# Performance work log

Hardware: AMD Instinct MI355X
Metric: run time of the kernel (lower is better)

Reference implementation:

```python
import jax, jax.numpy as jnp
import numpy as np

NHEAD = 8
DILATED = 1


def setup_inputs() -> dict:
    key = jax.random.key(0)
    ks = jax.random.split(key, 5)
    bs, c, h, w, k = 2, 256, 128, 128, 8
    L = (h // 2) * (w // 2)
    return {
        "query": jax.random.normal(ks[0], (bs, c, h, w), jnp.float32),
        "key": jax.random.normal(ks[1], (bs, c, h, w), jnp.float32),
        "value": jax.random.normal(ks[2], (bs, c, h, w), jnp.float32),
        "topk_pos": jax.random.randint(ks[3], (bs, L, k, 2), 0, h // 2, dtype=jnp.int32).astype(jnp.int64),
        "rel_pos": jax.random.normal(ks[4], (bs, NHEAD, h, w, 4 * k), jnp.float32),
    }


def reference(query, key, value, topk_pos, rel_pos):
    bs, c, h0, w0 = query.shape
    h1, w1 = key.shape[2], key.shape[3]
    nh = NHEAD
    d = c // nh
    L = (h0 // 2) * (w0 // 2)
    k = topk_pos.shape[2]
    k4 = 4 * k

    # key/value: [b,c,h,w] -> [b, h1*w1, nh, d]
    kf = key.reshape(bs, c, h1 * w1).transpose(0, 2, 1).reshape(bs, h1 * w1, nh, d)
    vf = value.reshape(bs, c, h1 * w1).transpose(0, 2, 1).reshape(bs, h1 * w1, nh, d)

    # query grouped into 2x2 blocks: [b, L, 4, nh, d]
    q = query.reshape(bs, nh, d, h0 // 2, 2, w0 // 2, 2)
    q = q.transpose(0, 3, 5, 4, 6, 1, 2).reshape(bs, L, 4, nh, d)

    # build gather indices into flattened key grid (offsets by dilation)
    tp = topk_pos * 2                               # [b, L, k, 2]
    row, col = tp[..., 0], tp[..., 1]
    offs = [(0, 0), (0, DILATED), (DILATED, 0), (DILATED, DILATED)]
    idx = jnp.stack([(row + x) * w1 + (col + y) for x, y in offs], axis=3)  # [b,L,k,4]
    idx = jnp.clip(idx, 0, h1 * w1 - 1).reshape(bs, L, k4)

    def gather(tbl):  # tbl: [b, h1*w1, nh, d] -> [b, L, k4, nh, d]
        return jax.vmap(lambda t, i: t[i])(tbl, idx.reshape(bs, L * k4)).reshape(bs, L, k4, nh, d)

    kg = gather(kf)
    vg = gather(vf)

    scale = 1.0 / np.sqrt(d).astype(np.float32)
    qk = jnp.einsum('blthd,blmhd->bltmh', q, kg) * scale  # [b,L,4,k4,nh]

    rp = rel_pos.reshape(bs, nh, h0 // 2, 2, w0 // 2, 2, k4)
    rp = rp.transpose(0, 2, 4, 3, 5, 6, 1).reshape(bs, L, 4, k4, nh)
    qk = qk + rp

    A = jax.nn.softmax(qk, axis=-2)  # softmax over the k*4 candidate axis
    msg = jnp.einsum('bltmh,blmhd->blthd', A, vg)  # [b,L,4,nh,d]

    # un-group 2x2 blocks back to full resolution: [b, h0*w0, c]
    msg = msg.reshape(bs, h0 // 2, w0 // 2, 2, 2, nh, d)
    msg = msg.transpose(0, 1, 3, 2, 4, 5, 6).reshape(bs, h0 * w0, c)

    up_idx = jnp.broadcast_to(idx[:, :, None, :], (bs, L, 4, k4))
    up_idx = up_idx.reshape(bs, h0 // 2, w0 // 2, 2, 2, k4)
    up_idx = up_idx.transpose(0, 1, 3, 2, 4, 5).reshape(bs, h0 * w0, k4)
    return msg, up_idx
```

## Files before the change

kernel.cpp:

```cpp
#include <hip/hip_runtime.h>
#include <hip/hip_fp16.h>
#include <math.h>

constexpr int NH = 8;
constexpr int D = 32;
constexpr int C = 256;
constexpr int H0 = 128;
constexpr int W0 = 128;
constexpr int PIX = H0 * W0;
constexpr int LBLK = 4096;
constexpr int K4 = 32;
constexpr int KSTH = 260;
constexpr int KST = 258;

typedef _Float16 half2_t __attribute__((ext_vector_type(2)));

#if defined(__has_builtin)
#if __has_builtin(__builtin_amdgcn_fdot2)
#define HAVE_FDOT2 1
#endif
#endif

__device__ __forceinline__ float fdot2_acc(half2_t a, half2_t b, float c) {
#ifdef HAVE_FDOT2
  return __builtin_amdgcn_fdot2(a, b, c, false);
#else
  return c + (float)a.x * (float)b.x + (float)a.y * (float)b.y;
#endif
}

__global__ __launch_bounds__(256) void transpose_qkv_kernel(
    const float* __restrict__ q, const float* __restrict__ k,
    const float* __restrict__ v, __half* __restrict__ qT,
    __half* __restrict__ kT, __half* __restrict__ vT)
{
  __shared__ float tile[64 * 65];
  const int z = blockIdx.z;
  const int b = z & 1;
  const int arr = z >> 1;
  const float* src = (arr == 0 ? q : arr == 1 ? k : v) + (size_t)b * C * PIX;
  __half* dst = (arr == 0 ? qT : arr == 1 ? kT : vT) + (size_t)b * PIX * C;

  const int p0 = blockIdx.x * 64;
  const int c0 = blockIdx.y * 64;
  const int t15 = threadIdx.x & 15;
  const int thi4 = threadIdx.x >> 4;

#pragma unroll
  for (int r = 0; r < 4; ++r) {
    const int ch = thi4 + r * 16;
    const int p4 = t15 * 4;
    float4 f = *(const float4*)&src[(size_t)(c0 + ch) * PIX + p0 + p4];
    tile[(p4 + 0) * 65 + ch] = f.x;
    tile[(p4 + 1) * 65 + ch] = f.y;
    tile[(p4 + 2) * 65 + ch] = f.z;
    tile[(p4 + 3) * 65 + ch] = f.w;
  }
  __syncthreads();

  const int t7 = threadIdx.x & 7;
  const int th8 = threadIdx.x >> 3;
#pragma unroll
  for (int r = 0; r < 2; ++r) {
    const int p = th8 + r * 32;
    const int c8 = t7 * 8;
    const float* tr = &tile[p * 65 + c8];
    __half2 h0 = __floats2half2_rn(tr[0], tr[1]);
    __half2 h1 = __floats2half2_rn(tr[2], tr[3]);
    __half2 h2 = __floats2half2_rn(tr[4], tr[5]);
    __half2 h3 = __floats2half2_rn(tr[6], tr[7]);
    uint4 u;
    u.x = *(unsigned*)&h0; u.y = *(unsigned*)&h1;
    u.z = *(unsigned*)&h2; u.w = *(unsigned*)&h3;
    *(uint4*)&dst[(size_t)(p0 + p) * C + c0 + c8] = u;
  }
}

__global__ __launch_bounds__(256) void cascade_attn_f16(
    const __half* __restrict__ qT,
    const __half* __restrict__ kT,
    const __half* __restrict__ vT,
    const int* __restrict__ topk,
    const float* __restrict__ relp,
    float* __restrict__ out_msg,
    float* __restrict__ out_idx)
{
  __shared__ __half kvh[K4 * KSTH];
  __shared__ __half qph[4 * C];

  const int tid = threadIdx.x;
  const int bid = blockIdx.x;
  const int b = bid >> 12;
  const int l = bid & (LBLK - 1);
  const int by = l >> 6, bx = l & 63;
  const int r0 = by * 2, c0 = bx * 2;

  const int* tp = topk + ((size_t)b * LBLK + l) * 16;

  const int h = tid >> 5;
  const int m = tid & 31;

  {
    const int t = tid >> 6, ln = tid & 63;
    const int pix = r0 * W0 + c0 + (t >> 1) * W0 + (t & 1);
    uint2 f = *(const uint2*)&qT[((size_t)b * PIX + pix) * C + ln * 4];
    *(uint2*)&qph[t * C + ln * 4] = f;
  }

  const int p = tid >> 3;
  const int ln8 = tid & 7;
  const int jj = p >> 2, o = p & 3;
  const int gpix = (tp[jj * 2] * 2 + (o >> 1)) * W0 + tp[jj * 2 + 1] * 2 + (o & 1);

  {
    const __half* src = &kT[((size_t)b * PIX + gpix) * C + ln8 * 8];
#pragma unroll
    for (int i = 0; i < 4; ++i) {
      uint4 f = *(const uint4*)(src + i * 64);
      __half* dst = &kvh[p * KSTH + ln8 * 8 + i * 64];
      *(uint2*)dst = make_uint2(f.x, f.y);
      *(uint2*)(dst + 4) = make_uint2(f.z, f.w);
    }
  }

  uint4 vreg[4];
  {
    const __half* src = &vT[((size_t)b * PIX + gpix) * C + ln8 * 8];
#pragma unroll
    for (int i = 0; i < 4; ++i) vreg[i] = *(const uint4*)(src + i * 64);
  }

  const size_t rb = ((((size_t)b * NH + h) * H0 + r0) * W0 + c0) * K4 + m;
  float rl0 = relp[rb];
  float rl1 = relp[rb + K4];
  float rl2 = relp[rb + (size_t)W0 * K4];
  float rl3 = relp[rb + (size_t)W0 * K4 + K4];

  if (tid < 128) {
    const int mm = tid & 31, t = tid >> 5;
    const int j2 = mm >> 2, o2 = mm & 3;
    const int pix = (tp[j2 * 2] * 2 + (o2 >> 1)) * W0 + tp[j2 * 2 + 1] * 2 + (o2 & 1);
    const int prow = r0 + (t >> 1), pcol = c0 + (t & 1);
    out_idx[((size_t)b * PIX + prow * W0 + pcol) * K4 + mm] = (float)pix;
  }
  __syncthreads();

  uint2 kw[8];
  {
    const __half* kbase = &kvh[m * KSTH + h * D];
#pragma unroll
    for (int i = 0; i < 8; ++i) kw[i] = *(const uint2*)(kbase + i * 4);
  }
  const half2_t* kh = (const half2_t*)kw;

  float acc[4] = {0.f, 0.f, 0.f, 0.f};
#pragma unroll
  for (int t = 0; t < 4; ++t) {
    uint4 qw[2];
    const uint4* qf = (const uint4*)&qph[t * C + h * D];
    qw[0] = qf[0];
    qw[1] = qf[1];
    const half2_t* qh2 = (const half2_t*)qw;
    uint4 qw2[2];
    qw2[0] = qf[2];
    qw2[1] = qf[3];
    const half2_t* qh2b = (const half2_t*)qw2;
#pragma unroll
    for (int i = 0; i < 8; ++i) acc[t] = fdot2_acc(qh2[i], kh[i], acc[t]);
#pragma unroll
    for (int i = 0; i < 8; ++i) acc[t] = fdot2_acc(qh2b[i], kh[8 + i], acc[t]);
  }

  const float scale = 0.17677669529663687f;
  float sv[4];
  sv[0] = acc[0] * scale + rl0;
  sv[1] = acc[1] * scale + rl1;
  sv[2] = acc[2] * scale + rl2;
  sv[3] = acc[3] * scale + rl3;

  float pr4[4];
#pragma unroll
  for (int t = 0; t < 4; ++t) {
    float x = sv[t];
    float mx = x;
#pragma unroll
    for (int off = 16; off > 0; off >>= 1) mx = fmaxf(mx, __shfl_xor(mx, off));
    float pbit = __expf(x - mx);
    float sm = pbit;
#pragma unroll
    for (int off = 16; off > 0; off >>= 1) sm += __shfl_xor(sm, off);
    pr4[t] = pbit / sm;
  }
  __syncthreads();

  {
    __half2 p01 = __floats2half2_rn(pr4[0], pr4[1]);
    __half2 p23 = __floats2half2_rn(pr4[2], pr4[3]);
    uint2 u;
    u.x = *(unsigned*)&p01;
    u.y = *(unsigned*)&p23;
    *(uint2*)&qph[tid * 4] = u;
  }
#pragma unroll
  for (int i = 0; i < 4; ++i) {
    __half* dst = &kvh[p * KSTH + ln8 * 8 + i * 64];
    *(uint2*)dst = make_uint2(vreg[i].x, vreg[i].y);
    *(uint2*)(dst + 4) = make_uint2(vreg[i].z, vreg[i].w);
  }
  __syncthreads();

  float o0 = 0.f, o1 = 0.f, o2 = 0.f, o3 = 0.f;
#pragma unroll
  for (int mm = 0; mm < 32; ++mm) {
    uint2 au = *(const uint2*)&qph[(h * K4 + mm) * 4];
    __half2 a01 = *(__half2*)&au.x;
    __half2 a23 = *(__half2*)&au.y;
    float2 f01 = __half22float2(a01);
    float2 f23 = __half22float2(a23);
    float vv = __half2float(kvh[mm * KSTH + h * D + m]);
    o0 += f01.x * vv;
    o1 += f01.y * vv;
    o2 += f23.x * vv;
    o3 += f23.y * vv;
  }
  const size_t ob = ((size_t)b * PIX + (size_t)r0 * W0 + c0) * C + h * D + m;
  out_msg[ob] = o0;
  out_msg[ob + C] = o1;
  out_msg[ob + (size_t)W0 * C] = o2;
  out_msg[ob + (size_t)W0 * C + C] = o3;
}

__global__ __launch_bounds__(256) void cascade_attn_fallback(
    const float* __restrict__ query, const float* __restrict__ key,
    const float* __restrict__ value, const int* __restrict__ topk,
    const float* __restrict__ relp, float* __restrict__ out_msg,
    float* __restrict__ out_idx)
{
  __shared__ float kv[K4 * KST];
  __shared__ float qs[4 * C];
  __shared__ float as_[NH * K4 * 4];

  const int tid = threadIdx.x;
  const int bid = blockIdx.x;
  const int b = bid >> 12;
  const int l = bid & (LBLK - 1);
  const int by = l >> 6, bx = l & 63;
  const int r0 = by * 2, c0 = bx * 2;

  const size_t plane = (size_t)PIX;
  const float* qb = query + (size_t)b * C * plane;
  const float* kb = key + (size_t)b * C * plane;
  const float* vb = value + (size_t)b * C * plane;
  const int* tp = topk + ((size_t)b * LBLK + l) * 16;

  {
    const float* qp = qb + (size_t)tid * plane + r0 * W0 + c0;
    float2 a = *(const float2*)qp;
    float2 bb = *(const float2*)(qp + W0);
    qs[0 * C + tid] = a.x; qs[1 * C + tid] = a.y;
    qs[2 * C + tid] = bb.x; qs[3 * C + tid] = bb.y;
  }
#pragma unroll
  for (int it = 0; it < 16; ++it) {
    const int jj = it >> 1, x = it & 1;
    const int pr = tp[jj * 2] * 2 + x;
    const int pc = tp[jj * 2 + 1] * 2;
    float2 f = *(const float2*)(kb + (size_t)tid * plane + pr * W0 + pc);
    const int m0 = jj * 4 + x * 2;
    kv[m0 * KST + tid] = f.x;
    kv[(m0 + 1) * KST + tid] = f.y;
  }
  if (tid < 128) {
    const int m = tid & 31, t = tid >> 5;
    const int jj = m >> 2, o = m & 3;
    const int pix = (tp[jj * 2] * 2 + (o >> 1)) * W0 + tp[jj * 2 + 1] * 2 + (o & 1);
    const int prow = r0 + (t >> 1), pcol = c0 + (t & 1);
    out_idx[((size_t)b * plane + prow * W0 + pcol) * K4 + m] = (float)pix;
  }
  __syncthreads();

  const int h = tid >> 5;
  const int m = tid & 31;
  float a0 = 0.f, a1 = 0.f, a2 = 0.f, a3 = 0.f;
#pragma unroll
  for (int dq = 0; dq < 8; ++dq) {
    const int off = h * D + dq * 4;
    float4 q0 = *(const float4*)&qs[0 * C + off];
    float4 q1 = *(const float4*)&qs[1 * C + off];
    float4 q2 = *(const float4*)&qs[2 * C + off];
    float4 q3 = *(const float4*)&qs[3 * C + off];
    float2 ka = *(const float2*)&kv[m * KST + off];
    float2 kc = *(const float2*)&kv[m * KST + off + 2];
    a0 += q0.x * ka.x + q0.y * ka.y + q0.z * kc.x + q0.w * kc.y;
    a1 += q1.x * ka.x + q1.y * ka.y + q1.z * kc.x + q1.w * kc.y;
    a2 += q2.x * ka.x + q2.y * ka.y + q2.z * kc.x + q2.w * kc.y;
    a3 += q3.x * ka.x + q3.y * ka.y + q3.z * kc.x + q3.w * kc.y;
  }
  const float scale = 0.17677669529663687f;
  const size_t rb = ((((size_t)b * NH + h) * H0 + r0) * W0 + c0) * K4 + m;
  float sv[4];
  sv[0] = a0 * scale + relp[rb];
  sv[1] = a1 * scale + relp[rb + K4];
  sv[2] = a2 * scale + relp[rb + (size_t)W0 * K4];
  sv[3] = a3 * scale + relp[rb + (size_t)W0 * K4 + K4];
  float pr4[4];
#pragma unroll
  for (int t = 0; t < 4; ++t) {
    float x = sv[t];
    float mx = x;
#pragma unroll
    for (int off = 16; off > 0; off >>= 1) mx = fmaxf(mx, __shfl_xor(mx, off));
    float pbit = __expf(x - mx);
    float sm = pbit;
#pragma unroll
    for (int off = 16; off > 0; off >>= 1) sm += __shfl_xor(sm, off);
    pr4[t] = pbit / sm;
  }
  *(float4*)&as_[tid * 4] = make_float4(pr4[0], pr4[1], pr4[2], pr4[3]);
  __syncthreads();
#pragma unroll
  for (int it = 0; it < 16; ++it) {
    const int jj = it >> 1, x = it & 1;
    const int pr = tp[jj * 2] * 2 + x;
    const int pc = tp[jj * 2 + 1] * 2;
    float2 f = *(const float2*)(vb + (size_t)tid * plane + pr * W0 + pc);
    const int m0 = jj * 4 + x * 2;
    kv[m0 * KST + tid] = f.x;
    kv[(m0 + 1) * KST + tid] = f.y;
  }
  __syncthreads();
  float o0 = 0.f, o1 = 0.f, o2 = 0.f, o3 = 0.f;
#pragma unroll
  for (int mm = 0; mm < 32; ++mm) {
    float4 a4 = *(const float4*)&as_[(h * K4 + mm) * 4];
    float vv = kv[mm * KST + h * D + m];
    o0 += a4.x * vv; o1 += a4.y * vv; o2 += a4.z * vv; o3 += a4.w * vv;
  }
  const size_t ob = ((size_t)b * plane + (size_t)r0 * W0 + c0) * C + h * D + m;
  out_msg[ob] = o0;
  out_msg[ob + C] = o1;
  out_msg[ob + (size_t)W0 * C] = o2;
  out_msg[ob + (size_t)W0 * C + C] = o3;
}

extern "C" void kernel_launch(void* const* d_in, const int* in_sizes, int n_in,
                              void* d_out, int out_size, void* d_ws, size_t ws_size,
                              hipStream_t stream) {
  const float* q = (const float*)d_in[0];
  const float* k = (const float*)d_in[1];
  const float* v = (const float*)d_in[2];
  const int* tp = (const int*)d_in[3];
  const float* rp = (const float*)d_in[4];

  float* out_msg = (float*)d_out;
  float* out_idx = out_msg + (size_t)2 * PIX * C;

  const size_t n_elem = (size_t)2 * PIX * C;
  const size_t needed = 3 * n_elem * sizeof(__half);
  if (ws_size >= needed) {
    __half* qT = (__half*)d_ws;
    __half* kT = qT + n_elem;
    __half* vT = kT + n_elem;
    dim3 tg(PIX / 64, C / 64, 6);
    hipLaunchKernelGGL(transpose_qkv_kernel, tg, dim3(256), 0, stream,
                       q, k, v, qT, kT, vT);
    hipLaunchKernelGGL(cascade_attn_f16, dim3(2 * LBLK), dim3(256), 0, stream,
                       qT, kT, vT, tp, rp, out_msg, out_idx);
  } else {
    hipLaunchKernelGGL(cascade_attn_fallback, dim3(2 * LBLK), dim3(256), 0, stream,
                       q, k, v, tp, rp, out_msg, out_idx);
  }
}
```

Measured before the change: 201.9 us.

## Use transposed LDS reads and fdot2 for the attention-times-V stage

The V tile is now stored in shared memory in a new 16-element-tiled layout and read back with the ds_read_b64_tr_b16 transpose instruction. Each thread then holds 16 candidate values for its channel, and probabilities are laid out per head and position so the weighted sum uses packed fp16 dot products instead of 32 scalar multiply-adds. This cuts LDS read count and ALU work in the second matmul. It also raises the launch-bounds occupancy hint and relies on gfx950-specific inline assembly whose lane mapping must match the chosen layout.

```diff
diff --git a/kernel.cpp b/kernel.cpp
--- a/kernel.cpp
+++ b/kernel.cpp
@@ -11,9 +11,11 @@
 constexpr int LBLK = 4096;
 constexpr int K4 = 32;
 constexpr int KSTH = 260;
+constexpr int VTS = 72;
 constexpr int KST = 258;
 
 typedef _Float16 half2_t __attribute__((ext_vector_type(2)));
+typedef unsigned u32x2 __attribute__((ext_vector_type(2)));
 
 #if defined(__has_builtin)
 #if __has_builtin(__builtin_amdgcn_fdot2)
@@ -27,6 +29,13 @@
 #else
   return c + (float)a.x * (float)b.x + (float)a.y * (float)b.y;
 #endif
+}
+
+__device__ __forceinline__ u32x2 ds_read_tr_b16(const __half* p) {
+  u32x2 r;
+  unsigned a = (unsigned)(unsigned long long)p;
+  asm volatile("ds_read_b64_tr_b16 %0, %1" : "=v"(r) : "v"(a));
+  return r;
 }
 
 __global__ __launch_bounds__(256) void transpose_qkv_kernel(
@@ -76,7 +85,7 @@
   }
 }
 
-__global__ __launch_bounds__(256) void cascade_attn_f16(
+__global__ __launch_bounds__(256, 8) void cascade_attn_f16(
     const __half* __restrict__ qT,
     const __half* __restrict__ kT,
     const __half* __restrict__ vT,
@@ -85,7 +94,7 @@
     float* __restrict__ out_msg,
     float* __restrict__ out_idx)
 {
-  __shared__ __half kvh[K4 * KSTH];
+  __shared__ __half kvh[128 * VTS];
   __shared__ __half qph[4 * C];
 
   const int tid = threadIdx.x;
@@ -109,8 +118,8 @@
 
   const int p = tid >> 3;
   const int ln8 = tid & 7;
-  const int jj = p >> 2, o = p & 3;
-  const int gpix = (tp[jj * 2] * 2 + (o >> 1)) * W0 + tp[jj * 2 + 1] * 2 + (o & 1);
+  const int jj = p >> 2, po = p & 3;
+  const int gpix = (tp[jj * 2] * 2 + (po >> 1)) * W0 + tp[jj * 2 + 1] * 2 + (po & 1);
 
   {
     const __half* src = &kT[((size_t)b * PIX + gpix) * C + ln8 * 8];
@@ -193,41 +202,54 @@
   }
   __syncthreads();
 
-  {
-    __half2 p01 = __floats2half2_rn(pr4[0], pr4[1]);
-    __half2 p23 = __floats2half2_rn(pr4[2], pr4[3]);
-    uint2 u;
-    u.x = *(unsigned*)&p01;
-    u.y = *(unsigned*)&p23;
-    *(uint2*)&qph[tid * 4] = u;
-  }
+#pragma unroll
+  for (int t = 0; t < 4; ++t)
+    qph[h * 128 + t * 32 + m] = __float2half(pr4[t]);
+
 #pragma unroll
   for (int i = 0; i < 4; ++i) {
-    __half* dst = &kvh[p * KSTH + ln8 * 8 + i * 64];
-    *(uint2*)dst = make_uint2(vreg[i].x, vreg[i].y);
-    *(uint2*)(dst + 4) = make_uint2(vreg[i].z, vreg[i].w);
-  }
-  __syncthreads();
-
-  float o0 = 0.f, o1 = 0.f, o2 = 0.f, o3 = 0.f;
-#pragma unroll
-  for (int mm = 0; mm < 32; ++mm) {
-    uint2 au = *(const uint2*)&qph[(h * K4 + mm) * 4];
-    __half2 a01 = *(__half2*)&au.x;
-    __half2 a23 = *(__half2*)&au.y;
-    float2 f01 = __half22float2(a01);
-    float2 f23 = __half22float2(a23);
-    float vv = __half2float(kvh[mm * KSTH + h * D + m]);
-    o0 += f01.x * vv;
-    o1 += f01.y * vv;
-    o2 += f23.x * vv;
-    o3 += f23.y * vv;
-  }
+    const int T = (p >> 2) * 16 + (ln8 >> 1) + i * 4;
+    __half* dst = &kvh[T * VTS + (p & 3) * 16 + (ln8 & 1) * 8];
+    *(uint4*)dst = vreg[i];
+  }
+  __syncthreads();
+
+  const int cb = (h * D + m) >> 4;
+  const int cin = m & 15;
+  u32x2 vtr[8];
+#pragma unroll
+  for (int g = 0; g < 8; ++g)
+    vtr[g] = ds_read_tr_b16(&kvh[(g * 16 + cb) * VTS + cin]);
+  asm volatile("s_waitcnt lgkmcnt(0)" ::: "memory");
+  __builtin_amdgcn_sched_barrier(0);
+
+  float oacc[4];
+#pragma unroll
+  for (int t = 0; t < 4; ++t) {
+    unsigned pw[8];
+    {
+      const uint4* pp = (const uint4*)&qph[h * 128 + t * 32];
+      uint4 A = pp[0], B = pp[1];
+      pw[0] = A.x; pw[1] = A.y; pw[2] = A.z; pw[3] = A.w;
+      pw[4] = B.x; pw[5] = B.y; pw[6] = B.z; pw[7] = B.w;
+    }
+    float s = 0.f;
+#pragma unroll
+    for (int g = 0; g < 8; ++g) {
+      unsigned vlo = vtr[g][0], vhi = vtr[g][1];
+      s = fdot2_acc(__builtin_bit_cast(half2_t, pw[2 * g]),
+                    __builtin_bit_cast(half2_t, vlo), s);
+      s = fdot2_acc(__builtin_bit_cast(half2_t, pw[2 * g + 1]),
+                    __builtin_bit_cast(half2_t, vhi), s);
+    }
+    oacc[t] = s;
+  }
+
   const size_t ob = ((size_t)b * PIX + (size_t)r0 * W0 + c0) * C + h * D + m;
-  out_msg[ob] = o0;
-  out_msg[ob + C] = o1;
-  out_msg[ob + (size_t)W0 * C] = o2;
-  out_msg[ob + (size_t)W0 * C + C] = o3;
+  out_msg[ob] = oacc[0];
+  out_msg[ob + C] = oacc[1];
+  out_msg[ob + (size_t)W0 * C] = oacc[2];
+  out_msg[ob + (size_t)W0 * C + C] = oacc[3];
 }
 
 __global__ __launch_bounds__(256) void cascade_attn_fallback(
```

Result: slower. 248.5 us (+23.1%).

## Load K and Q directly to registers and use fdot2 for the PV product

Applied to the files above, without the earlier changes.

Each thread now reads its gathered key row and the query rows straight from global memory into registers, so K no longer goes through shared memory and the Q staging and two barriers are removed. V is written to shared memory with full 16-byte stores and a new padded stride. Probabilities are stored interleaved so the PV accumulation can use packed fdot2 over pairs of candidates. Launch bounds request 8 blocks per CU. The cost is redundant global loads of Q across the 32 lanes of each head and higher register pressure under the tighter occupancy hint.

```diff
diff --git a/kernel.cpp b/kernel.cpp
--- a/kernel.cpp
+++ b/kernel.cpp
@@ -10,7 +10,7 @@
 constexpr int PIX = H0 * W0;
 constexpr int LBLK = 4096;
 constexpr int K4 = 32;
-constexpr int KSTH = 260;
+constexpr int VST = 264;
 constexpr int KST = 258;
 
 typedef _Float16 half2_t __attribute__((ext_vector_type(2)));
@@ -76,7 +76,7 @@
   }
 }
 
-__global__ __launch_bounds__(256) void cascade_attn_f16(
+__global__ __launch_bounds__(256, 8) void cascade_attn_f16(
     const __half* __restrict__ qT,
     const __half* __restrict__ kT,
     const __half* __restrict__ vT,
@@ -85,8 +85,8 @@
     float* __restrict__ out_msg,
     float* __restrict__ out_idx)
 {
-  __shared__ __half kvh[K4 * KSTH];
-  __shared__ __half qph[4 * C];
+  __shared__ __half vsh[K4 * VST];
+  __shared__ __half pph[NH * 128];
 
   const int tid = threadIdx.x;
   const int bid = blockIdx.x;
@@ -100,34 +100,27 @@
   const int h = tid >> 5;
   const int m = tid & 31;
 
+  const int gm = (tp[(m >> 2) * 2] * 2 + ((m & 3) >> 1)) * W0 +
+                 tp[(m >> 2) * 2 + 1] * 2 + (m & 1);
+
+  uint4 kw4[4];
   {
-    const int t = tid >> 6, ln = tid & 63;
-    const int pix = r0 * W0 + c0 + (t >> 1) * W0 + (t & 1);
-    uint2 f = *(const uint2*)&qT[((size_t)b * PIX + pix) * C + ln * 4];
-    *(uint2*)&qph[t * C + ln * 4] = f;
+    const uint4* kptr = (const uint4*)&kT[((size_t)b * PIX + gm) * C + h * D];
+#pragma unroll
+    for (int i = 0; i < 4; ++i) kw4[i] = kptr[i];
   }
 
   const int p = tid >> 3;
   const int ln8 = tid & 7;
-  const int jj = p >> 2, o = p & 3;
-  const int gpix = (tp[jj * 2] * 2 + (o >> 1)) * W0 + tp[jj * 2 + 1] * 2 + (o & 1);
-
   {
-    const __half* src = &kT[((size_t)b * PIX + gpix) * C + ln8 * 8];
+    const int jj = p >> 2, po = p & 3;
+    const int gp = (tp[jj * 2] * 2 + (po >> 1)) * W0 + tp[jj * 2 + 1] * 2 + (po & 1);
+    const __half* src = &vT[((size_t)b * PIX + gp) * C + ln8 * 8];
 #pragma unroll
     for (int i = 0; i < 4; ++i) {
       uint4 f = *(const uint4*)(src + i * 64);
-      __half* dst = &kvh[p * KSTH + ln8 * 8 + i * 64];
-      *(uint2*)dst = make_uint2(f.x, f.y);
-      *(uint2*)(dst + 4) = make_uint2(f.z, f.w);
+      *(uint4*)&vsh[p * VST + ln8 * 8 + i * 64] = f;
     }
-  }
-
-  uint4 vreg[4];
-  {
-    const __half* src = &vT[((size_t)b * PIX + gpix) * C + ln8 * 8];
-#pragma unroll
-    for (int i = 0; i < 4; ++i) vreg[i] = *(const uint4*)(src + i * 64);
   }
 
   const size_t rb = ((((size_t)b * NH + h) * H0 + r0) * W0 + c0) * K4 + m;
@@ -143,32 +136,21 @@
     const int prow = r0 + (t >> 1), pcol = c0 + (t & 1);
     out_idx[((size_t)b * PIX + prow * W0 + pcol) * K4 + mm] = (float)pix;
   }
-  __syncthreads();
-
-  uint2 kw[8];
-  {
-    const __half* kbase = &kvh[m * KSTH + h * D];
-#pragma unroll
-    for (int i = 0; i < 8; ++i) kw[i] = *(const uint2*)(kbase + i * 4);
-  }
-  const half2_t* kh = (const half2_t*)kw;
-
-  float acc[4] = {0.f, 0.f, 0.f, 0.f};
+
+  const half2_t* kh = (const half2_t*)kw4;
+  float acc[4];
 #pragma unroll
   for (int t = 0; t < 4; ++t) {
-    uint4 qw[2];
-    const uint4* qf = (const uint4*)&qph[t * C + h * D];
-    qw[0] = qf[0];
-    qw[1] = qf[1];
-    const half2_t* qh2 = (const half2_t*)qw;
-    uint4 qw2[2];
-    qw2[0] = qf[2];
-    qw2[1] = qf[3];
-    const half2_t* qh2b = (const half2_t*)qw2;
-#pragma unroll
-    for (int i = 0; i < 8; ++i) acc[t] = fdot2_acc(qh2[i], kh[i], acc[t]);
-#pragma unroll
-    for (int i = 0; i < 8; ++i) acc[t] = fdot2_acc(qh2b[i], kh[8 + i], acc[t]);
+    const int pix = (r0 + (t >> 1)) * W0 + c0 + (t & 1);
+    const uint4* qptr = (const uint4*)&qT[((size_t)b * PIX + pix) * C + h * D];
+    uint4 qw4[4];
+#pragma unroll
+    for (int i = 0; i < 4; ++i) qw4[i] = qptr[i];
+    const half2_t* qh = (const half2_t*)qw4;
+    float s = 0.f;
+#pragma unroll
+    for (int i = 0; i < 16; ++i) s = fdot2_acc(qh[i], kh[i], s);
+    acc[t] = s;
   }
 
   const float scale = 0.17677669529663687f;
@@ -191,38 +173,31 @@
     for (int off = 16; off > 0; off >>= 1) sm += __shfl_xor(sm, off);
     pr4[t] = pbit / sm;
   }
-  __syncthreads();
 
   {
-    __half2 p01 = __floats2half2_rn(pr4[0], pr4[1]);
-    __half2 p23 = __floats2half2_rn(pr4[2], pr4[3]);
-    uint2 u;
-    u.x = *(unsigned*)&p01;
-    u.y = *(unsigned*)&p23;
-    *(uint2*)&qph[tid * 4] = u;
-  }
-#pragma unroll
-  for (int i = 0; i < 4; ++i) {
-    __half* dst = &kvh[p * KSTH + ln8 * 8 + i * 64];
-    *(uint2*)dst = make_uint2(vreg[i].x, vreg[i].y);
-    *(uint2*)(dst + 4) = make_uint2(vreg[i].z, vreg[i].w);
+    const int d = m >> 1, lohi = m & 1;
+#pragma unroll
+    for (int t = 0; t < 4; ++t)
+      pph[h * 128 + d * 8 + t * 2 + lohi] = __float2half(pr4[t]);
   }
   __syncthreads();
 
   float o0 = 0.f, o1 = 0.f, o2 = 0.f, o3 = 0.f;
-#pragma unroll
-  for (int mm = 0; mm < 32; ++mm) {
-    uint2 au = *(const uint2*)&qph[(h * K4 + mm) * 4];
-    __half2 a01 = *(__half2*)&au.x;
-    __half2 a23 = *(__half2*)&au.y;
-    float2 f01 = __half22float2(a01);
-    float2 f23 = __half22float2(a23);
-    float vv = __half2float(kvh[mm * KSTH + h * D + m]);
-    o0 += f01.x * vv;
-    o1 += f01.y * vv;
-    o2 += f23.x * vv;
-    o3 += f23.y * vv;
-  }
+  const uint4* pp = (const uint4*)&pph[h * 128];
+  const __half* vcol = &vsh[h * D + m];
+#pragma unroll
+  for (int d = 0; d < 16; ++d) {
+    uint4 u = pp[d];
+    __half vlo = vcol[(2 * d) * VST];
+    __half vhi = vcol[(2 * d + 1) * VST];
+    __half2 vp2 = __halves2half2(vlo, vhi);
+    half2_t vp = __builtin_bit_cast(half2_t, vp2);
+    o0 = fdot2_acc(__builtin_bit_cast(half2_t, u.x), vp, o0);
+    o1 = fdot2_acc(__builtin_bit_cast(half2_t, u.y), vp, o1);
+    o2 = fdot2_acc(__builtin_bit_cast(half2_t, u.z), vp, o2);
+    o3 = fdot2_acc(__builtin_bit_cast(half2_t, u.w), vp, o3);
+  }
+
   const size_t ob = ((size_t)b * PIX + (size_t)r0 * W0 + c0) * C + h * D + m;
   out_msg[ob] = o0;
   out_msg[ob + C] = o1;
```

Result: slower. 232.4 us (+15.1%).
